# Performance work log

Hardware: AMD Instinct MI355X
Metric: run time of the kernel (lower is better)

The kernel has to match this reference:

```python
import jax, jax.numpy as jnp
import numpy as np

SINKHORN_ITERS = 20
EPS = 1e-6


def sinkhorn(M, n_iter=SINKHORN_ITERS, eps=EPS):
    # Project (n, n) logits onto the Birkhoff polytope (doubly stochastic).
    A = jnp.exp(M - jnp.max(M, axis=(-2, -1), keepdims=True))
    for _ in range(n_iter):
        A = A / (A.sum(axis=-1, keepdims=True) + eps)
        A = A / (A.sum(axis=-2, keepdims=True) + eps)
    return A


def setup_inputs() -> dict:
    key = jax.random.key(0)
    k1, k2, k3, k4 = jax.random.split(key, 4)
    B, S, D, E = 4, 4096, 4096, 4
    return {
        "x": jax.random.normal(k1, (B, S, D), dtype=jnp.float32),
        "H_res_logits": jax.random.normal(k2, (E, E), dtype=jnp.float32),
        "H_pre_logits": jax.random.normal(k3, (E, D), dtype=jnp.float32),
        "H_post_logits": jax.random.normal(k4, (E, D), dtype=jnp.float32),
    }


def reference(x, H_res_logits, H_pre_logits, H_post_logits):
    # MHCLayer forward with layer=None (residual routing only), sinkhorn projection.
    H_res = sinkhorn(H_res_logits)                      # (E, E) doubly stochastic
    H_pre = jax.nn.softmax(H_pre_logits, axis=-1)       # (E, D)
    H_post = jax.nn.softmax(H_post_logits, axis=-1)     # (E, D)

    # x_pre = (x.unsqueeze(-2) * H_pre).sum(-1)  ==  x @ H_pre^T
    x_pre = jnp.einsum("bsd,ed->bse", x, H_pre)         # (B, S, E)
    out_exp = x_pre @ H_res                             # (B, S, E)
    # out = (out_exp.unsqueeze(-1) * H_post).sum(-2)  ==  out_exp @ H_post
    out = jnp.einsum("bse,ed->bsd", out_exp, H_post)    # (B, S, D)
    return out
```

## Files before the change

kernel.cpp:

```cpp
#include <hip/hip_runtime.h>
#include <math.h>

#define E 4
#define TPB 256
#define RPB 8
#define NWAVES (TPB / 64)
#define SINKHORN_ITERS 20
#define SINKHORN_EPS 1e-6f

typedef float f4 __attribute__((ext_vector_type(4)));


__global__ __launch_bounds__(TPB) void prep_stats(
    const float* __restrict__ Hres_l,
    const float* __restrict__ Hpre_l,
    const float* __restrict__ Hpost_l,
    float* __restrict__ ws_small,
    int D4)
{
    const int t = threadIdx.x;
    const int wave = t >> 6;
    const int lane = t & 63;

    if (wave == 0) {
        float a = (lane < E * E) ? Hres_l[lane] : -1e30f;
        float m = a;
#pragma unroll
        for (int off = 1; off < 16; off <<= 1)
            m = fmaxf(m, __shfl_xor(m, off, 16));
        a = expf(a - m);
        for (int it = 0; it < SINKHORN_ITERS; ++it) {
            float rs = a;
            rs += __shfl_xor(rs, 1, 4);
            rs += __shfl_xor(rs, 2, 4);
            a /= (rs + SINKHORN_EPS);
            float cs = a;
            cs += __shfl_xor(cs, 4, 16);
            cs += __shfl_xor(cs, 8, 16);
            a /= (cs + SINKHORN_EPS);
        }
        if (lane < E * E) ws_small[lane] = a;
    }

    for (int pi = 0; pi < 2; ++pi) {
        const int p = wave * 2 + pi;
        const int mat = p >> 2, e = p & 3;
        const f4* rowp = (const f4*)((mat ? Hpost_l : Hpre_l) + (size_t)e * D4 * 4);
        float m = -1e30f;
        for (int i = lane; i < D4; i += 64) {
            f4 v = rowp[i];
            m = fmaxf(fmaxf(fmaxf(m, v.x), v.y), fmaxf(v.z, v.w));
        }
#pragma unroll
        for (int off = 1; off < 64; off <<= 1)
            m = fmaxf(m, __shfl_xor(m, off, 64));
        float s = 0.f;
        for (int i = lane; i < D4; i += 64) {
            f4 v = rowp[i];
            s += expf(v.x - m) + expf(v.y - m) + expf(v.z - m) + expf(v.w - m);
        }
#pragma unroll
        for (int off = 1; off < 64; off <<= 1)
            s += __shfl_xor(s, off, 64);
        if (lane == 0) { ws_small[16 + p] = m; ws_small[24 + p] = s; }
    }
}

__global__ __launch_bounds__(TPB) void prep_write(
    const float* __restrict__ Hpre_l,
    const float* __restrict__ Hpost_l,
    const float* __restrict__ ws_small,
    f4* __restrict__ wpre4,
    f4* __restrict__ wpost4,
    int D4)
{
    const int i = blockIdx.x * TPB + threadIdx.x;
    if (i >= D4) return;

    float hres[E * E];
#pragma unroll
    for (int k = 0; k < E * E; ++k) hres[k] = ws_small[k];
    float mpre[E], spre[E], mpost[E], spost[E];
#pragma unroll
    for (int e = 0; e < E; ++e) {
        mpre[e]  = ws_small[16 + e];     spre[e]  = 1.f / ws_small[24 + e];
        mpost[e] = ws_small[16 + E + e]; spost[e] = 1.f / ws_small[24 + E + e];
    }

    const f4* pre_l4  = (const f4*)Hpre_l;
    const f4* post_l4 = (const f4*)Hpost_l;
    f4 postv[E];
#pragma unroll
    for (int e = 0; e < E; ++e) {
        f4 v = pre_l4[(size_t)e * D4 + i];
        f4 o;
        o.x = expf(v.x - mpre[e]) * spre[e];
        o.y = expf(v.y - mpre[e]) * spre[e];
        o.z = expf(v.z - mpre[e]) * spre[e];
        o.w = expf(v.w - mpre[e]) * spre[e];
        wpre4[(size_t)e * D4 + i] = o;
        f4 w = post_l4[(size_t)e * D4 + i];
        postv[e].x = expf(w.x - mpost[e]) * spost[e];
        postv[e].y = expf(w.y - mpost[e]) * spost[e];
        postv[e].z = expf(w.z - mpost[e]) * spost[e];
        postv[e].w = expf(w.w - mpost[e]) * spost[e];
    }
#pragma unroll
    for (int ep = 0; ep < E; ++ep) {
        f4 o = hres[ep * E + 0] * postv[0] + hres[ep * E + 1] * postv[1] +
               hres[ep * E + 2] * postv[2] + hres[ep * E + 3] * postv[3];
        wpost4[(size_t)ep * D4 + i] = o;
    }
}

__global__ __launch_bounds__(TPB) void xpre_kernel(
    const f4* __restrict__ x4,
    const f4* __restrict__ pre4,
    float* __restrict__ xpre,
    int D4, int chunks)
{
    __shared__ float wred[NWAVES][RPB * E];
    const int t = threadIdx.x;
    const int wave = t >> 6;
    const int lane = t & 63;
    const long row0 = (long)blockIdx.x * RPB;

    float val[RPB * E];
#pragma unroll
    for (int i = 0; i < RPB * E; ++i) val[i] = 0.f;

    for (int k = 0; k < chunks; ++k) {
        const int d4 = k * TPB + t;
        f4 hp[E];
#pragma unroll
        for (int e = 0; e < E; ++e) hp[e] = pre4[(size_t)e * D4 + d4];
#pragma unroll
        for (int r = 0; r < RPB; ++r) {
            f4 xv = __builtin_nontemporal_load(&x4[(row0 + r) * D4 + d4]);
#pragma unroll
            for (int e = 0; e < E; ++e)
                val[r * E + e] += xv.x * hp[e].x + xv.y * hp[e].y +
                                  xv.z * hp[e].z + xv.w * hp[e].w;
        }
    }

    {
        const bool h0 = lane & 1;
        float a16[16];
#pragma unroll
        for (int i = 0; i < 16; ++i) {
            float send = h0 ? val[2 * i] : val[2 * i + 1];
            float recv = __shfl_xor(send, 1, 64);
            a16[i] = (h0 ? val[2 * i + 1] : val[2 * i]) + recv;
        }
        const bool h1 = (lane >> 1) & 1;
        float a8[8];
#pragma unroll
        for (int i = 0; i < 8; ++i) {
            float send = h1 ? a16[2 * i] : a16[2 * i + 1];
            float recv = __shfl_xor(send, 2, 64);
            a8[i] = (h1 ? a16[2 * i + 1] : a16[2 * i]) + recv;
        }
        const bool h2 = (lane >> 2) & 1;
        float a4[4];
#pragma unroll
        for (int i = 0; i < 4; ++i) {
            float send = h2 ? a8[2 * i] : a8[2 * i + 1];
            float recv = __shfl_xor(send, 4, 64);
            a4[i] = (h2 ? a8[2 * i + 1] : a8[2 * i]) + recv;
        }
        const bool h3 = (lane >> 3) & 1;
        float a2[2];
#pragma unroll
        for (int i = 0; i < 2; ++i) {
            float send = h3 ? a4[2 * i] : a4[2 * i + 1];
            float recv = __shfl_xor(send, 8, 64);
            a2[i] = (h3 ? a4[2 * i + 1] : a4[2 * i]) + recv;
        }
        const bool h4 = (lane >> 4) & 1;
        float send = h4 ? a2[0] : a2[1];
        float recv = __shfl_xor(send, 16, 64);
        float a1 = (h4 ? a2[1] : a2[0]) + recv;
        a1 += __shfl_xor(a1, 32, 64);
        if (lane < 32) wred[wave][lane] = a1;
    }
    __syncthreads();

    if (t < RPB * E) {
        float s = wred[0][t] + wred[1][t] + wred[2][t] + wred[3][t];
        const int r = t >> 2, e = t & 3;
        xpre[(row0 + r) * E + e] = s;
    }
}

__global__ __launch_bounds__(TPB) void out_kernel(
    const float* __restrict__ xpre,
    const f4* __restrict__ post4,
    f4* __restrict__ out4,
    int D4, int chunks)
{
    __shared__ float sxp[RPB * E];
    const int t = threadIdx.x;
    const long row0 = (long)blockIdx.x * RPB;

    if (t < RPB * E) sxp[t] = xpre[row0 * E + t];
    __syncthreads();

    float xp[RPB][E];
#pragma unroll
    for (int r = 0; r < RPB; ++r)
#pragma unroll
        for (int e = 0; e < E; ++e) xp[r][e] = sxp[r * E + e];

    for (int k = 0; k < chunks; ++k) {
        const int d4 = k * TPB + t;
        f4 hq[E];
#pragma unroll
        for (int e = 0; e < E; ++e) hq[e] = post4[(size_t)e * D4 + d4];
#pragma unroll
        for (int r = 0; r < RPB; ++r) {
            f4 o = xp[r][0] * hq[0] + xp[r][1] * hq[1] +
                   xp[r][2] * hq[2] + xp[r][3] * hq[3];
            __builtin_nontemporal_store(o, &out4[(row0 + r) * D4 + d4]);
        }
    }
}

extern "C" void kernel_launch(void* const* d_in, const int* in_sizes, int n_in,
                              void* d_out, int out_size, void* d_ws, size_t ws_size,
                              hipStream_t stream) {
    const float* x     = (const float*)d_in[0];
    const float* Hres  = (const float*)d_in[1];
    const float* Hpre  = (const float*)d_in[2];
    const float* Hpost = (const float*)d_in[3];
    float* out = (float*)d_out;

    const int D = in_sizes[2] / E;
    const long rows = (long)in_sizes[0] / D;
    const int D4 = D / 4;
    const int chunks = D4 / TPB;

    float* ws_pre   = (float*)d_ws;
    float* ws_post2 = ws_pre + (size_t)E * D;
    float* ws_small = ws_post2 + (size_t)E * D;
    float* ws_xpre  = ws_small + 32;

    prep_stats<<<1, TPB, 0, stream>>>(Hres, Hpre, Hpost, ws_small, D4);
    prep_write<<<(D4 + TPB - 1) / TPB, TPB, 0, stream>>>(
        Hpre, Hpost, ws_small, (f4*)ws_pre, (f4*)ws_post2, D4);

    const int grid = (int)(rows / RPB);
    xpre_kernel<<<grid, TPB, 0, stream>>>((const f4*)x, (const f4*)ws_pre,
                                          ws_xpre, D4, chunks);
    out_kernel<<<grid, TPB, 0, stream>>>(ws_xpre, (const f4*)ws_post2,
                                         (f4*)out, D4, chunks);
}
```

Measured before the change: 122.2 us.

## Fuse softmax and Sinkhorn preprocessing into the two main streaming kernels

Removes the two prep kernels and has every block recompute the softmax max and denominator for H_pre and H_post from the raw logits. The H_pre normalisation is folded into a final division of the accumulated dot products, and Sinkhorn plus the H_res mix are applied to the per-row x_pre values. This saves two launches and the workspace round trip, at the cost of redundant per-block max/sum passes over the (E, D) logits and many more exp evaluations in the hot loops.

```diff
diff --git a/kernel.cpp b/kernel.cpp
--- a/kernel.cpp
+++ b/kernel.cpp
@@ -11,19 +11,149 @@
 typedef float f4 __attribute__((ext_vector_type(4)));
 
 
-__global__ __launch_bounds__(TPB) void prep_stats(
-    const float* __restrict__ Hres_l,
-    const float* __restrict__ Hpre_l,
-    const float* __restrict__ Hpost_l,
-    float* __restrict__ ws_small,
-    int D4)
+__global__ __launch_bounds__(TPB) void xpre_osm(
+    const f4* __restrict__ x4,
+    const f4* __restrict__ preL4,
+    float* __restrict__ xpre,
+    int D4, int chunks)
 {
+    __shared__ float redm[NWAVES][E];
+    __shared__ float sden[NWAVES][E];
+    __shared__ float wred[NWAVES][RPB * E];
     const int t = threadIdx.x;
     const int wave = t >> 6;
     const int lane = t & 63;
+    const long row0 = (long)blockIdx.x * RPB;
+
+    float mx[E];
+#pragma unroll
+    for (int e = 0; e < E; ++e) mx[e] = -1e30f;
+    for (int k = 0; k < chunks; ++k) {
+        const int i = k * TPB + t;
+#pragma unroll
+        for (int e = 0; e < E; ++e) {
+            f4 v = preL4[(size_t)e * D4 + i];
+            mx[e] = fmaxf(mx[e], fmaxf(fmaxf(v.x, v.y), fmaxf(v.z, v.w)));
+        }
+    }
+#pragma unroll
+    for (int e = 0; e < E; ++e) {
+        float m = mx[e];
+#pragma unroll
+        for (int off = 1; off < 64; off <<= 1)
+            m = fmaxf(m, __shfl_xor(m, off, 64));
+        if (lane == 0) redm[wave][e] = m;
+    }
+    __syncthreads();
+#pragma unroll
+    for (int e = 0; e < E; ++e)
+        mx[e] = fmaxf(fmaxf(redm[0][e], redm[1][e]),
+                      fmaxf(redm[2][e], redm[3][e]));
+
+    float num[RPB * E];
+#pragma unroll
+    for (int i = 0; i < RPB * E; ++i) num[i] = 0.f;
+    float den[E] = {0.f, 0.f, 0.f, 0.f};
+
+    for (int k = 0; k < chunks; ++k) {
+        const int i = k * TPB + t;
+        f4 hp[E];
+#pragma unroll
+        for (int e = 0; e < E; ++e) {
+            f4 v = preL4[(size_t)e * D4 + i];
+            hp[e].x = expf(v.x - mx[e]);
+            hp[e].y = expf(v.y - mx[e]);
+            hp[e].z = expf(v.z - mx[e]);
+            hp[e].w = expf(v.w - mx[e]);
+            den[e] += hp[e].x + hp[e].y + hp[e].z + hp[e].w;
+        }
+#pragma unroll
+        for (int r = 0; r < RPB; ++r) {
+            f4 xv = __builtin_nontemporal_load(&x4[(row0 + r) * D4 + i]);
+#pragma unroll
+            for (int e = 0; e < E; ++e)
+                num[r * E + e] += xv.x * hp[e].x + xv.y * hp[e].y +
+                                  xv.z * hp[e].z + xv.w * hp[e].w;
+        }
+    }
+
+#pragma unroll
+    for (int e = 0; e < E; ++e) {
+        float v = den[e];
+#pragma unroll
+        for (int off = 1; off < 64; off <<= 1) v += __shfl_xor(v, off, 64);
+        if (lane == 0) sden[wave][e] = v;
+    }
+
+    {
+        const bool h0 = lane & 1;
+        float a16[16];
+#pragma unroll
+        for (int i = 0; i < 16; ++i) {
+            float send = h0 ? num[2 * i] : num[2 * i + 1];
+            float recv = __shfl_xor(send, 1, 64);
+            a16[i] = (h0 ? num[2 * i + 1] : num[2 * i]) + recv;
+        }
+        const bool h1 = (lane >> 1) & 1;
+        float a8[8];
+#pragma unroll
+        for (int i = 0; i < 8; ++i) {
+            float send = h1 ? a16[2 * i] : a16[2 * i + 1];
+            float recv = __shfl_xor(send, 2, 64);
+            a8[i] = (h1 ? a16[2 * i + 1] : a16[2 * i]) + recv;
+        }
+        const bool h2 = (lane >> 2) & 1;
+        float a4[4];
+#pragma unroll
+        for (int i = 0; i < 4; ++i) {
+            float send = h2 ? a8[2 * i] : a8[2 * i + 1];
+            float recv = __shfl_xor(send, 4, 64);
+            a4[i] = (h2 ? a8[2 * i + 1] : a8[2 * i]) + recv;
+        }
+        const bool h3 = (lane >> 3) & 1;
+        float a2[2];
+#pragma unroll
+        for (int i = 0; i < 2; ++i) {
+            float send = h3 ? a4[2 * i] : a4[2 * i + 1];
+            float recv = __shfl_xor(send, 8, 64);
+            a2[i] = (h3 ? a4[2 * i + 1] : a4[2 * i]) + recv;
+        }
+        const bool h4 = (lane >> 4) & 1;
+        float send = h4 ? a2[0] : a2[1];
+        float recv = __shfl_xor(send, 16, 64);
+        float a1 = (h4 ? a2[1] : a2[0]) + recv;
+        a1 += __shfl_xor(a1, 32, 64);
+        if (lane < 32) wred[wave][lane] = a1;
+    }
+    __syncthreads();
+
+    if (t < RPB * E) {
+        const int e = t & 3;
+        float numtot = wred[0][t] + wred[1][t] + wred[2][t] + wred[3][t];
+        float dentot = sden[0][e] + sden[1][e] + sden[2][e] + sden[3][e];
+        const int r = t >> 2;
+        xpre[(row0 + r) * E + e] = numtot / dentot;
+    }
+}
+
+__global__ __launch_bounds__(TPB) void out_osm(
+    const float* __restrict__ xpre,
+    const f4* __restrict__ postL4,
+    const float* __restrict__ HresL,
+    f4* __restrict__ out4,
+    int D4, int chunks)
+{
+    __shared__ float sHres[E * E];
+    __shared__ float sxp[RPB * E];
+    __shared__ float redm[NWAVES][E];
+    __shared__ float sden[NWAVES][E];
+    const int t = threadIdx.x;
+    const int wave = t >> 6;
+    const int lane = t & 63;
+    const long row0 = (long)blockIdx.x * RPB;
 
     if (wave == 0) {
-        float a = (lane < E * E) ? Hres_l[lane] : -1e30f;
+        float a = (lane < E * E) ? HresL[lane] : -1e30f;
         float m = a;
 #pragma unroll
         for (int off = 1; off < 16; off <<= 1)
@@ -39,189 +169,85 @@
             cs += __shfl_xor(cs, 8, 16);
             a /= (cs + SINKHORN_EPS);
         }
-        if (lane < E * E) ws_small[lane] = a;
-    }
-
-    for (int pi = 0; pi < 2; ++pi) {
-        const int p = wave * 2 + pi;
-        const int mat = p >> 2, e = p & 3;
-        const f4* rowp = (const f4*)((mat ? Hpost_l : Hpre_l) + (size_t)e * D4 * 4);
-        float m = -1e30f;
-        for (int i = lane; i < D4; i += 64) {
-            f4 v = rowp[i];
-            m = fmaxf(fmaxf(fmaxf(m, v.x), v.y), fmaxf(v.z, v.w));
-        }
+        if (lane < E * E) sHres[lane] = a;
+    }
+    if (t >= 64 && t < 64 + RPB * E) sxp[t - 64] = xpre[row0 * E + (t - 64)];
+
+    float mx[E];
+#pragma unroll
+    for (int e = 0; e < E; ++e) mx[e] = -1e30f;
+    for (int k = 0; k < chunks; ++k) {
+        const int i = k * TPB + t;
+#pragma unroll
+        for (int e = 0; e < E; ++e) {
+            f4 v = postL4[(size_t)e * D4 + i];
+            mx[e] = fmaxf(mx[e], fmaxf(fmaxf(v.x, v.y), fmaxf(v.z, v.w)));
+        }
+    }
+#pragma unroll
+    for (int e = 0; e < E; ++e) {
+        float m = mx[e];
 #pragma unroll
         for (int off = 1; off < 64; off <<= 1)
             m = fmaxf(m, __shfl_xor(m, off, 64));
-        float s = 0.f;
-        for (int i = lane; i < D4; i += 64) {
-            f4 v = rowp[i];
-            s += expf(v.x - m) + expf(v.y - m) + expf(v.z - m) + expf(v.w - m);
-        }
-#pragma unroll
-        for (int off = 1; off < 64; off <<= 1)
-            s += __shfl_xor(s, off, 64);
-        if (lane == 0) { ws_small[16 + p] = m; ws_small[24 + p] = s; }
-    }
-}
-
-__global__ __launch_bounds__(TPB) void prep_write(
-    const float* __restrict__ Hpre_l,
-    const float* __restrict__ Hpost_l,
-    const float* __restrict__ ws_small,
-    f4* __restrict__ wpre4,
-    f4* __restrict__ wpost4,
-    int D4)
-{
-    const int i = blockIdx.x * TPB + threadIdx.x;
-    if (i >= D4) return;
-
-    float hres[E * E];
-#pragma unroll
-    for (int k = 0; k < E * E; ++k) hres[k] = ws_small[k];
-    float mpre[E], spre[E], mpost[E], spost[E];
-#pragma unroll
-    for (int e = 0; e < E; ++e) {
-        mpre[e]  = ws_small[16 + e];     spre[e]  = 1.f / ws_small[24 + e];
-        mpost[e] = ws_small[16 + E + e]; spost[e] = 1.f / ws_small[24 + E + e];
-    }
-
-    const f4* pre_l4  = (const f4*)Hpre_l;
-    const f4* post_l4 = (const f4*)Hpost_l;
-    f4 postv[E];
-#pragma unroll
-    for (int e = 0; e < E; ++e) {
-        f4 v = pre_l4[(size_t)e * D4 + i];
-        f4 o;
-        o.x = expf(v.x - mpre[e]) * spre[e];
-        o.y = expf(v.y - mpre[e]) * spre[e];
-        o.z = expf(v.z - mpre[e]) * spre[e];
-        o.w = expf(v.w - mpre[e]) * spre[e];
-        wpre4[(size_t)e * D4 + i] = o;
-        f4 w = post_l4[(size_t)e * D4 + i];
-        postv[e].x = expf(w.x - mpost[e]) * spost[e];
-        postv[e].y = expf(w.y - mpost[e]) * spost[e];
-        postv[e].z = expf(w.z - mpost[e]) * spost[e];
-        postv[e].w = expf(w.w - mpost[e]) * spost[e];
-    }
-#pragma unroll
-    for (int ep = 0; ep < E; ++ep) {
-        f4 o = hres[ep * E + 0] * postv[0] + hres[ep * E + 1] * postv[1] +
-               hres[ep * E + 2] * postv[2] + hres[ep * E + 3] * postv[3];
-        wpost4[(size_t)ep * D4 + i] = o;
-    }
-}
-
-__global__ __launch_bounds__(TPB) void xpre_kernel(
-    const f4* __restrict__ x4,
-    const f4* __restrict__ pre4,
-    float* __restrict__ xpre,
-    int D4, int chunks)
-{
-    __shared__ float wred[NWAVES][RPB * E];
-    const int t = threadIdx.x;
-    const int wave = t >> 6;
-    const int lane = t & 63;
-    const long row0 = (long)blockIdx.x * RPB;
-
-    float val[RPB * E];
-#pragma unroll
-    for (int i = 0; i < RPB * E; ++i) val[i] = 0.f;
-
-    for (int k = 0; k < chunks; ++k) {
-        const int d4 = k * TPB + t;
-        f4 hp[E];
-#pragma unroll
-        for (int e = 0; e < E; ++e) hp[e] = pre4[(size_t)e * D4 + d4];
+        if (lane == 0) redm[wave][e] = m;
+    }
+    __syncthreads();
+#pragma unroll
+    for (int e = 0; e < E; ++e)
+        mx[e] = fmaxf(fmaxf(redm[0][e], redm[1][e]),
+                      fmaxf(redm[2][e], redm[3][e]));
+
+    float den[E] = {0.f, 0.f, 0.f, 0.f};
+    for (int k = 0; k < chunks; ++k) {
+        const int i = k * TPB + t;
+#pragma unroll
+        for (int e = 0; e < E; ++e) {
+            f4 v = postL4[(size_t)e * D4 + i];
+            den[e] += expf(v.x - mx[e]) + expf(v.y - mx[e]) +
+                      expf(v.z - mx[e]) + expf(v.w - mx[e]);
+        }
+    }
+#pragma unroll
+    for (int e = 0; e < E; ++e) {
+        float v = den[e];
+#pragma unroll
+        for (int off = 1; off < 64; off <<= 1) v += __shfl_xor(v, off, 64);
+        if (lane == 0) sden[wave][e] = v;
+    }
+    __syncthreads();
+
+    float xp2[RPB][E];
+#pragma unroll
+    for (int e = 0; e < E; ++e) {
+        float d = sden[0][e] + sden[1][e] + sden[2][e] + sden[3][e];
+        float inv = 1.f / d;
 #pragma unroll
         for (int r = 0; r < RPB; ++r) {
-            f4 xv = __builtin_nontemporal_load(&x4[(row0 + r) * D4 + d4]);
-#pragma unroll
-            for (int e = 0; e < E; ++e)
-                val[r * E + e] += xv.x * hp[e].x + xv.y * hp[e].y +
-                                  xv.z * hp[e].z + xv.w * hp[e].w;
-        }
-    }
-
-    {
-        const bool h0 = lane & 1;
-        float a16[16];
-#pragma unroll
-        for (int i = 0; i < 16; ++i) {
-            float send = h0 ? val[2 * i] : val[2 * i + 1];
-            float recv = __shfl_xor(send, 1, 64);
-            a16[i] = (h0 ? val[2 * i + 1] : val[2 * i]) + recv;
-        }
-        const bool h1 = (lane >> 1) & 1;
-        float a8[8];
-#pragma unroll
-        for (int i = 0; i < 8; ++i) {
-            float send = h1 ? a16[2 * i] : a16[2 * i + 1];
-            float recv = __shfl_xor(send, 2, 64);
-            a8[i] = (h1 ? a16[2 * i + 1] : a16[2 * i]) + recv;
-        }
-        const bool h2 = (lane >> 2) & 1;
-        float a4[4];
-#pragma unroll
-        for (int i = 0; i < 4; ++i) {
-            float send = h2 ? a8[2 * i] : a8[2 * i + 1];
-            float recv = __shfl_xor(send, 4, 64);
-            a4[i] = (h2 ? a8[2 * i + 1] : a8[2 * i]) + recv;
-        }
-        const bool h3 = (lane >> 3) & 1;
-        float a2[2];
-#pragma unroll
-        for (int i = 0; i < 2; ++i) {
-            float send = h3 ? a4[2 * i] : a4[2 * i + 1];
-            float recv = __shfl_xor(send, 8, 64);
-            a2[i] = (h3 ? a4[2 * i + 1] : a4[2 * i]) + recv;
-        }
-        const bool h4 = (lane >> 4) & 1;
-        float send = h4 ? a2[0] : a2[1];
-        float recv = __shfl_xor(send, 16, 64);
-        float a1 = (h4 ? a2[1] : a2[0]) + recv;
-        a1 += __shfl_xor(a1, 32, 64);
-        if (lane < 32) wred[wave][lane] = a1;
-    }
-    __syncthreads();
-
-    if (t < RPB * E) {
-        float s = wred[0][t] + wred[1][t] + wred[2][t] + wred[3][t];
-        const int r = t >> 2, e = t & 3;
-        xpre[(row0 + r) * E + e] = s;
-    }
-}
-
-__global__ __launch_bounds__(TPB) void out_kernel(
-    const float* __restrict__ xpre,
-    const f4* __restrict__ post4,
-    f4* __restrict__ out4,
-    int D4, int chunks)
-{
-    __shared__ float sxp[RPB * E];
-    const int t = threadIdx.x;
-    const long row0 = (long)blockIdx.x * RPB;
-
-    if (t < RPB * E) sxp[t] = xpre[row0 * E + t];
-    __syncthreads();
-
-    float xp[RPB][E];
-#pragma unroll
-    for (int r = 0; r < RPB; ++r)
-#pragma unroll
-        for (int e = 0; e < E; ++e) xp[r][e] = sxp[r * E + e];
-
-    for (int k = 0; k < chunks; ++k) {
-        const int d4 = k * TPB + t;
-        f4 hq[E];
-#pragma unroll
-        for (int e = 0; e < E; ++e) hq[e] = post4[(size_t)e * D4 + d4];
+            float acc = sxp[r * E + 0] * sHres[0 * E + e] +
+                        sxp[r * E + 1] * sHres[1 * E + e] +
+                        sxp[r * E + 2] * sHres[2 * E + e] +
+                        sxp[r * E + 3] * sHres[3 * E + e];
+            xp2[r][e] = acc * inv;
+        }
+    }
+
+    for (int k = 0; k < chunks; ++k) {
+        const int i = k * TPB + t;
+        f4 hv[E];
+#pragma unroll
+        for (int e = 0; e < E; ++e) {
+            f4 v = postL4[(size_t)e * D4 + i];
+            hv[e].x = expf(v.x - mx[e]);
+            hv[e].y = expf(v.y - mx[e]);
+            hv[e].z = expf(v.z - mx[e]);
+            hv[e].w = expf(v.w - mx[e]);
+        }
 #pragma unroll
         for (int r = 0; r < RPB; ++r) {
-            f4 o = xp[r][0] * hq[0] + xp[r][1] * hq[1] +
-                   xp[r][2] * hq[2] + xp[r][3] * hq[3];
-            __builtin_nontemporal_store(o, &out4[(row0 + r) * D4 + d4]);
+            f4 o = xp2[r][0] * hv[0] + xp2[r][1] * hv[1] +
+                   xp2[r][2] * hv[2] + xp2[r][3] * hv[3];
+            __builtin_nontemporal_store(o, &out4[(row0 + r) * D4 + i]);
         }
     }
 }
@@ -240,18 +266,11 @@
     const int D4 = D / 4;
     const int chunks = D4 / TPB;
 
-    float* ws_pre   = (float*)d_ws;
-    float* ws_post2 = ws_pre + (size_t)E * D;
-    float* ws_small = ws_post2 + (size_t)E * D;
-    float* ws_xpre  = ws_small + 32;
-
-    prep_stats<<<1, TPB, 0, stream>>>(Hres, Hpre, Hpost, ws_small, D4);
-    prep_write<<<(D4 + TPB - 1) / TPB, TPB, 0, stream>>>(
-        Hpre, Hpost, ws_small, (f4*)ws_pre, (f4*)ws_post2, D4);
+    float* ws_xpre = (float*)d_ws;
 
     const int grid = (int)(rows / RPB);
-    xpre_kernel<<<grid, TPB, 0, stream>>>((const f4*)x, (const f4*)ws_pre,
-                                          ws_xpre, D4, chunks);
-    out_kernel<<<grid, TPB, 0, stream>>>(ws_xpre, (const f4*)ws_post2,
-                                         (f4*)out, D4, chunks);
+    xpre_osm<<<grid, TPB, 0, stream>>>((const f4*)x, (const f4*)Hpre,
+                                       ws_xpre, D4, chunks);
+    out_osm<<<grid, TPB, 0, stream>>>(ws_xpre, (const f4*)Hpost, Hres,
+                                      (f4*)out, D4, chunks);
 }
```

After: 127.2 us. 1.04x slower.
